# Optimization experiments

Measured on AMD Instinct MI355X. Metric: run time of the kernel, lower is better.

Reference implementation:

```python
import jax, jax.numpy as jnp
import numpy as np

IN, OUT, FP, B, S = 8192, 28672, 128, 32, 1


def setup_inputs() -> dict:
    key = jax.random.key(0)
    k = jax.random.split(key, 6)
    x = jax.random.normal(k[0], (B, S, IN), dtype=jnp.float32).astype(jnp.float16)
    # int8 quantized weight, stored as [OUT, IN]
    weight = jax.random.randint(k[1], (OUT, IN), -128, 128, dtype=jnp.int32).astype(jnp.int8)
    # per-output-column dequant scale (fp16, positive, small)
    scale_col = (jax.random.uniform(k[2], (1, OUT), dtype=jnp.float32) * 0.01 + 1e-4).astype(jnp.float16)
    # fp16 cache of the outlier weight columns [OUT, FP]
    weight_cache = (jax.random.normal(k[3], (OUT, FP), dtype=jnp.float32) * 0.02).astype(jnp.float16)
    bias = (jax.random.normal(k[4], (OUT,), dtype=jnp.float32) * 0.02).astype(jnp.float16)
    # sorted unique outlier column indices
    ind = jnp.sort(jax.random.permutation(k[5], IN)[:FP]).astype(jnp.int32)
    return {"x": x, "weight": weight, "scale_col": scale_col,
            "weight_cache": weight_cache, "bias": bias, "ind": ind}


def reference(x, weight, scale_col, weight_cache, bias, ind):
    out_features = weight.shape[0]
    shape = x.shape[:-1] + (out_features,)
    inputs = x.reshape(-1, x.shape[-1])                       # [M, IN] fp16
    # ExtractOutliersAndSetToZeros: gather outlier activation columns, zero them
    act_outliers = inputs[:, ind]                              # [M, FP] fp16
    tmp = inputs.at[:, ind].set(jnp.float16(0))                # [M, IN]
    # FindRowScale (bit=8): symmetric per-row int8 scale
    x_scale = jnp.max(jnp.abs(tmp), axis=1, keepdims=True) / jnp.float16(127)  # [M, 1]
    q_x = jnp.clip(jnp.round(tmp / x_scale), -128, 127).astype(jnp.int8)       # [M, IN]
    # int8FusedDequantize: int8 GEMM -> dequant with row/col scales -> add fp16 outlier GEMM
    y_int = jnp.matmul(q_x.astype(jnp.int32), weight.T.astype(jnp.int32))      # [M, OUT] int32
    y = y_int.astype(jnp.float16) * x_scale * scale_col                        # dequantize
    y = y + jnp.matmul(act_outliers, weight_cache.T)                           # outlier fp16 GEMM
    y = y + bias
    return y.reshape(shape)
```

## Files before the change

kernel.cpp:

```cpp
#include <hip/hip_runtime.h>
#include <hip/hip_fp16.h>

#define IN_F   8192
#define OUT_F  28672
#define NFP    128
#define NB     32
#define KQTOT  (IN_F / 4)

#define WS_QPK 0
#define WS_XS  262144
#define WS_ACT 263168

typedef int v4i  __attribute__((ext_vector_type(4)));
typedef int v16i __attribute__((ext_vector_type(16)));

__device__ __forceinline__ int pack8(int4 v) {
    return (v.x & 0xFF) | ((v.y & 0xFF) << 8) | ((v.z & 0xFF) << 16) | (v.w << 24);
}

__global__ __launch_bounds__(256) void quant_kernel(
    const float* __restrict__ x, const int* __restrict__ ind,
    int* __restrict__ q_pk, float* __restrict__ xs_out,
    float* __restrict__ act_out)
{
    __shared__ unsigned char flags[IN_F];
    __shared__ float redbuf[4];
    __shared__ float xs_sh;
    const int tid = threadIdx.x;
    const int b = blockIdx.x;

    int* fl4 = (int*)flags;
    for (int i = tid; i < IN_F / 4; i += 256) fl4[i] = 0;
    __syncthreads();
    if (tid < NFP) flags[ind[tid]] = 1;
    __syncthreads();

    const float* xrow = x + (size_t)b * IN_F;
    const float4* x4 = (const float4*)xrow;
    float mx = 0.f;
    for (int c = tid; c < IN_F / 4; c += 256) {
        float4 v = x4[c];
        int fw = fl4[c];
        if (!(fw & 0x000000FF)) mx = fmaxf(mx, fabsf(v.x));
        if (!(fw & 0x0000FF00)) mx = fmaxf(mx, fabsf(v.y));
        if (!(fw & 0x00FF0000)) mx = fmaxf(mx, fabsf(v.z));
        if (!(fw & 0xFF000000)) mx = fmaxf(mx, fabsf(v.w));
    }
    #pragma unroll
    for (int off = 32; off > 0; off >>= 1) {
        float o = __shfl_down(mx, off, 64);
        mx = o > mx ? o : mx;
    }
    if ((tid & 63) == 0) redbuf[tid >> 6] = mx;
    __syncthreads();
    if (tid == 0) {
        float m = redbuf[0];
        #pragma unroll
        for (int i = 1; i < 4; i++) m = redbuf[i] > m ? redbuf[i] : m;
        float xs = __half2float(__float2half_rn(m / 127.0f));
        xs_sh = xs;
        xs_out[b] = xs;
    }
    __syncthreads();
    const float xs = xs_sh;

    for (int c = tid; c < IN_F / 4; c += 256) {
        float4 v = x4[c];
        int fw = fl4[c];
        float ee[4];
        ee[0] = (fw & 0x000000FF) ? 0.f : v.x;
        ee[1] = (fw & 0x0000FF00) ? 0.f : v.y;
        ee[2] = (fw & 0x00FF0000) ? 0.f : v.z;
        ee[3] = (fw & 0xFF000000) ? 0.f : v.w;
        int pk = 0;
        #pragma unroll
        for (int j = 0; j < 4; j++) {
            float qf = __half2float(__float2half_rn(ee[j] / xs));
            float r = rintf(qf);
            r = fminf(fmaxf(r, -128.f), 127.f);
            int qi = (int)r;
            pk |= (qi & 0xFF) << (8 * j);
        }
        q_pk[(size_t)b * KQTOT + c] = pk;
    }
    if (tid < NFP) act_out[b * NFP + tid] = xrow[ind[tid]];
}

#define OT   64
#define KT   256
#define KQT  (KT / 4)
#define WROW 68
#define QROW 68

__global__ __launch_bounds__(128) void gemm_kernel(
    const int* __restrict__ w, const int* __restrict__ q_pk,
    const float* __restrict__ xs_ws, const float* __restrict__ act_ws,
    const float* __restrict__ sc, const float* __restrict__ wc,
    const float* __restrict__ bias, float* __restrict__ out)
{
    __shared__ int   w_p[OT * WROW] __attribute__((aligned(16)));
    __shared__ int   q_t[NB * QROW] __attribute__((aligned(16)));
    __shared__ float act_l[NB * NFP];
    __shared__ float xs_l[NB];

    const int tid  = threadIdx.x;
    const int wave = tid >> 6;
    const int lane = tid & 63;
    const int nl   = lane & 31;
    const int half = lane >> 5;

    const int blk_o = blockIdx.x * OT;
    const int n = blk_o + wave * 32 + nl;

    for (int i = tid; i < NB * NFP; i += 128) act_l[i] = act_ws[i];
    if (tid < NB) xs_l[tid] = xs_ws[tid];

    v16i acc;
    #pragma unroll
    for (int r = 0; r < 16; r++) acc[r] = 0;

    for (int k0 = 0; k0 < IN_F; k0 += KT) {
        __syncthreads();
        #pragma unroll 4
        for (int i = 0; i < 8; i++) {
            int u  = i * 128 + tid;
            int r  = u >> 4;
            int c4 = u & 15;
            const int* src = w + (size_t)(blk_o + r) * IN_F + k0 + c4 * 16;
            int4 a = *(const int4*)(src + 0);
            int4 b = *(const int4*)(src + 4);
            int4 c = *(const int4*)(src + 8);
            int4 d = *(const int4*)(src + 12);
            int4 pk = make_int4(pack8(a), pack8(b), pack8(c), pack8(d));
            *(int4*)&w_p[r * WROW + c4 * 4] = pk;
        }
        #pragma unroll
        for (int i = 0; i < 4; i++) {
            int u  = i * 128 + tid;
            int b  = u >> 4;
            int c4 = u & 15;
            int4 v = *(const int4*)(q_pk + (size_t)b * KQTOT + (k0 >> 2) + c4 * 4);
            *(int4*)&q_t[b * QROW + c4 * 4] = v;
        }
        __syncthreads();

        const int* qrow = &q_t[nl * QROW + half * 4];
        const int* wrow = &w_p[(wave * 32 + nl) * WROW + half * 4];
        #pragma unroll
        for (int s = 0; s < KT / 32; s++) {
            v4i a = *(const v4i*)(qrow + s * 8);
            v4i b = *(const v4i*)(wrow + s * 8);
            acc = __builtin_amdgcn_mfma_i32_32x32x32_i8(a, b, acc, 0, 0, 0);
        }
    }

    const float scn = sc[n];
    const float bin = bias[n];
    const float* wcn = wc + (size_t)n * NFP;

    float dots[16];
    #pragma unroll
    for (int r = 0; r < 16; r++) dots[r] = 0.f;

    for (int j = 0; j < NFP; j += 4) {
        float4 wv = *(const float4*)(wcn + j);
        #pragma unroll
        for (int r = 0; r < 16; r++) {
            int b = (r & 3) + 8 * (r >> 2) + 4 * half;
            float4 av = *(const float4*)(&act_l[b * NFP + j]);
            dots[r] += av.x * wv.x + av.y * wv.y + av.z * wv.z + av.w * wv.w;
        }
    }

    #pragma unroll
    for (int r = 0; r < 16; r++) {
        int b = (r & 3) + 8 * (r >> 2) + 4 * half;
        out[(size_t)b * OUT_F + n] = (float)acc[r] * xs_l[b] * scn + dots[r] + bin;
    }
}

extern "C" void kernel_launch(void* const* d_in, const int* in_sizes, int n_in,
                              void* d_out, int out_size, void* d_ws, size_t ws_size,
                              hipStream_t stream) {
    const float* x    = (const float*)d_in[0];
    const int*   wgt  = (const int*)d_in[1];
    const float* scol = (const float*)d_in[2];
    const float* wch  = (const float*)d_in[3];
    const float* bias = (const float*)d_in[4];
    const int*   ind  = (const int*)d_in[5];
    float* out = (float*)d_out;

    int*   q_pk = (int*)((char*)d_ws + WS_QPK);
    float* xs   = (float*)((char*)d_ws + WS_XS);
    float* act  = (float*)((char*)d_ws + WS_ACT);

    quant_kernel<<<NB, 256, 0, stream>>>(x, ind, q_pk, xs, act);
    gemm_kernel<<<OUT_F / OT, 128, 0, stream>>>(wgt, q_pk, xs, act, scol, wch, bias, out);
}
```

Baseline: 1.194 ms.

## Split-K the int8 GEMM with double-buffered LDS and a separate epilogue kernel

Result: no change. 1.212 ms (+1.5%).

```diff
diff --git a/kernel.cpp b/kernel.cpp
--- a/kernel.cpp
+++ b/kernel.cpp
@@ -7,9 +7,13 @@
 #define NB     32
 #define KQTOT  (IN_F / 4)
 
-#define WS_QPK 0
-#define WS_XS  262144
-#define WS_ACT 263168
+#define KC     4
+#define KCHUNK (IN_F / KC)
+
+#define WS_QPK  0
+#define WS_XS   262144
+#define WS_ACT  263168
+#define WS_PART 524288
 
 typedef int v4i  __attribute__((ext_vector_type(4)));
 typedef int v16i __attribute__((ext_vector_type(16)));
@@ -86,22 +90,47 @@
     if (tid < NFP) act_out[b * NFP + tid] = xrow[ind[tid]];
 }
 
-#define OT   64
-#define KT   256
-#define KQT  (KT / 4)
-#define WROW 68
-#define QROW 68
+#define OT    64
+#define KT    256
+#define KQT   (KT / 4)
+#define WROW  68
+#define QROW  68
+#define NTILE (KCHUNK / KT)
+
+__device__ __forceinline__ void stage_tiles(
+    const int* __restrict__ w, const int* __restrict__ q_pk,
+    int* __restrict__ wp, int* __restrict__ qt,
+    int tid, int blk_o, int k0)
+{
+    #pragma unroll 4
+    for (int i = 0; i < 8; i++) {
+        int u  = i * 128 + tid;
+        int r  = u >> 4;
+        int c4 = u & 15;
+        const int* src = w + (size_t)(blk_o + r) * IN_F + k0 + c4 * 16;
+        int4 a = *(const int4*)(src + 0);
+        int4 b = *(const int4*)(src + 4);
+        int4 c = *(const int4*)(src + 8);
+        int4 d = *(const int4*)(src + 12);
+        int4 pk = make_int4(pack8(a), pack8(b), pack8(c), pack8(d));
+        *(int4*)&wp[r * WROW + c4 * 4] = pk;
+    }
+    #pragma unroll
+    for (int i = 0; i < 4; i++) {
+        int u  = i * 128 + tid;
+        int bb = u >> 4;
+        int c4 = u & 15;
+        int4 v = *(const int4*)(q_pk + (size_t)bb * KQTOT + (k0 >> 2) + c4 * 4);
+        *(int4*)&qt[bb * QROW + c4 * 4] = v;
+    }
+}
 
 __global__ __launch_bounds__(128) void gemm_kernel(
     const int* __restrict__ w, const int* __restrict__ q_pk,
-    const float* __restrict__ xs_ws, const float* __restrict__ act_ws,
-    const float* __restrict__ sc, const float* __restrict__ wc,
-    const float* __restrict__ bias, float* __restrict__ out)
-{
-    __shared__ int   w_p[OT * WROW] __attribute__((aligned(16)));
-    __shared__ int   q_t[NB * QROW] __attribute__((aligned(16)));
-    __shared__ float act_l[NB * NFP];
-    __shared__ float xs_l[NB];
+    int* __restrict__ part)
+{
+    __shared__ int w_p[2][OT * WROW] __attribute__((aligned(16)));
+    __shared__ int q_t[2][NB * QROW] __attribute__((aligned(16)));
 
     const int tid  = threadIdx.x;
     const int wave = tid >> 6;
@@ -109,73 +138,84 @@
     const int nl   = lane & 31;
     const int half = lane >> 5;
 
-    const int blk_o = blockIdx.x * OT;
+    const int kc    = blockIdx.x & (KC - 1);
+    const int blk_o = (blockIdx.x >> 2) * OT;
+    const int kbase = kc * KCHUNK;
     const int n = blk_o + wave * 32 + nl;
 
-    for (int i = tid; i < NB * NFP; i += 128) act_l[i] = act_ws[i];
-    if (tid < NB) xs_l[tid] = xs_ws[tid];
-
     v16i acc;
     #pragma unroll
     for (int r = 0; r < 16; r++) acc[r] = 0;
 
-    for (int k0 = 0; k0 < IN_F; k0 += KT) {
-        __syncthreads();
-        #pragma unroll 4
-        for (int i = 0; i < 8; i++) {
-            int u  = i * 128 + tid;
-            int r  = u >> 4;
-            int c4 = u & 15;
-            const int* src = w + (size_t)(blk_o + r) * IN_F + k0 + c4 * 16;
-            int4 a = *(const int4*)(src + 0);
-            int4 b = *(const int4*)(src + 4);
-            int4 c = *(const int4*)(src + 8);
-            int4 d = *(const int4*)(src + 12);
-            int4 pk = make_int4(pack8(a), pack8(b), pack8(c), pack8(d));
-            *(int4*)&w_p[r * WROW + c4 * 4] = pk;
-        }
-        #pragma unroll
-        for (int i = 0; i < 4; i++) {
-            int u  = i * 128 + tid;
-            int b  = u >> 4;
-            int c4 = u & 15;
-            int4 v = *(const int4*)(q_pk + (size_t)b * KQTOT + (k0 >> 2) + c4 * 4);
-            *(int4*)&q_t[b * QROW + c4 * 4] = v;
-        }
-        __syncthreads();
-
-        const int* qrow = &q_t[nl * QROW + half * 4];
-        const int* wrow = &w_p[(wave * 32 + nl) * WROW + half * 4];
+    stage_tiles(w, q_pk, w_p[0], q_t[0], tid, blk_o, kbase);
+    __syncthreads();
+
+    for (int t = 0; t < NTILE; ++t) {
+        const int cur = t & 1;
+        if (t + 1 < NTILE)
+            stage_tiles(w, q_pk, w_p[cur ^ 1], q_t[cur ^ 1],
+                        tid, blk_o, kbase + (t + 1) * KT);
+
+        const int* qrow = &q_t[cur][nl * QROW + half * 4];
+        const int* wrow = &w_p[cur][(wave * 32 + nl) * WROW + half * 4];
         #pragma unroll
         for (int s = 0; s < KT / 32; s++) {
             v4i a = *(const v4i*)(qrow + s * 8);
             v4i b = *(const v4i*)(wrow + s * 8);
             acc = __builtin_amdgcn_mfma_i32_32x32x32_i8(a, b, acc, 0, 0, 0);
         }
-    }
-
+        __syncthreads();
+    }
+
+    #pragma unroll
+    for (int r = 0; r < 16; r++) {
+        int b = (r & 3) + 8 * (r >> 2) + 4 * half;
+        part[((size_t)kc * NB + b) * OUT_F + n] = acc[r];
+    }
+}
+
+__global__ __launch_bounds__(256) void epilogue_kernel(
+    const int* __restrict__ part, const float* __restrict__ xs_ws,
+    const float* __restrict__ act_ws, const float* __restrict__ sc,
+    const float* __restrict__ wc, const float* __restrict__ bias,
+    float* __restrict__ out)
+{
+    __shared__ float act_l[NB * NFP];
+    __shared__ float xs_l[NB];
+    const int tid = threadIdx.x;
+    const int blk_o = blockIdx.x * 64;
+
+    for (int i = tid; i < NB * NFP; i += 256) act_l[i] = act_ws[i];
+    if (tid < NB) xs_l[tid] = xs_ws[tid];
+    __syncthreads();
+
+    const int nl = tid & 63;
+    const int n  = blk_o + nl;
+    const int b0 = (tid >> 6) * 8;
     const float scn = sc[n];
     const float bin = bias[n];
     const float* wcn = wc + (size_t)n * NFP;
 
-    float dots[16];
-    #pragma unroll
-    for (int r = 0; r < 16; r++) dots[r] = 0.f;
-
-    for (int j = 0; j < NFP; j += 4) {
-        float4 wv = *(const float4*)(wcn + j);
-        #pragma unroll
-        for (int r = 0; r < 16; r++) {
-            int b = (r & 3) + 8 * (r >> 2) + 4 * half;
-            float4 av = *(const float4*)(&act_l[b * NFP + j]);
-            dots[r] += av.x * wv.x + av.y * wv.y + av.z * wv.z + av.w * wv.w;
+    float dots[8];
+    #pragma unroll
+    for (int j = 0; j < 8; j++) dots[j] = 0.f;
+    for (int u = 0; u < NFP; u += 4) {
+        float4 wv = *(const float4*)(wcn + u);
+        #pragma unroll
+        for (int j = 0; j < 8; j++) {
+            float4 av = *(const float4*)(&act_l[(b0 + j) * NFP + u]);
+            dots[j] += av.x * wv.x + av.y * wv.y + av.z * wv.z + av.w * wv.w;
         }
     }
 
     #pragma unroll
-    for (int r = 0; r < 16; r++) {
-        int b = (r & 3) + 8 * (r >> 2) + 4 * half;
-        out[(size_t)b * OUT_F + n] = (float)acc[r] * xs_l[b] * scn + dots[r] + bin;
+    for (int j = 0; j < 8; j++) {
+        const int b = b0 + j;
+        const size_t idx = (size_t)b * OUT_F + n;
+        int s = part[idx];
+        #pragma unroll
+        for (int k = 1; k < KC; k++) s += part[((size_t)k * NB + b) * OUT_F + n];
+        out[idx] = (float)s * xs_l[b] * scn + dots[j] + bin;
     }
 }
 
@@ -193,7 +233,9 @@
     int*   q_pk = (int*)((char*)d_ws + WS_QPK);
     float* xs   = (float*)((char*)d_ws + WS_XS);
     float* act  = (float*)((char*)d_ws + WS_ACT);
+    int*   part = (int*)((char*)d_ws + WS_PART);
 
     quant_kernel<<<NB, 256, 0, stream>>>(x, ind, q_pk, xs, act);
-    gemm_kernel<<<OUT_F / OT, 128, 0, stream>>>(wgt, q_pk, xs, act, scol, wch, bias, out);
-}
+    gemm_kernel<<<(OUT_F / OT) * KC, 128, 0, stream>>>(wgt, q_pk, part);
+    epilogue_kernel<<<OUT_F / 64, 256, 0, stream>>>(part, xs, act, scol, wch, bias, out);
+}
```

## Split K across wave pairs with LDS reduction and larger K tile

Applied to the files above, without the earlier changes.

Result: no change. 1.204 ms (+0.8%).

```diff
diff --git a/kernel.cpp b/kernel.cpp
--- a/kernel.cpp
+++ b/kernel.cpp
@@ -7,9 +7,9 @@
 #define NB     32
 #define KQTOT  (IN_F / 4)
 
-#define WS_QPK 0
-#define WS_XS  262144
-#define WS_ACT 263168
+#define WS_QPK  0
+#define WS_XS   262144
+#define WS_ACT  263168
 
 typedef int v4i  __attribute__((ext_vector_type(4)));
 typedef int v16i __attribute__((ext_vector_type(16)));
@@ -86,96 +86,110 @@
     if (tid < NFP) act_out[b * NFP + tid] = xrow[ind[tid]];
 }
 
-#define OT   64
-#define KT   256
-#define KQT  (KT / 4)
-#define WROW 68
-#define QROW 68
-
-__global__ __launch_bounds__(128) void gemm_kernel(
+#define KT    512
+#define NT    (IN_F / KT)
+#define WROW  132
+#define QROW  132
+
+__global__ __launch_bounds__(256) void gemm_kernel(
     const int* __restrict__ w, const int* __restrict__ q_pk,
     const float* __restrict__ xs_ws, const float* __restrict__ act_ws,
     const float* __restrict__ sc, const float* __restrict__ wc,
     const float* __restrict__ bias, float* __restrict__ out)
 {
-    __shared__ int   w_p[OT * WROW] __attribute__((aligned(16)));
-    __shared__ int   q_t[NB * QROW] __attribute__((aligned(16)));
-    __shared__ float act_l[NB * NFP];
-    __shared__ float xs_l[NB];
+    __shared__ int w_p[64 * WROW] __attribute__((aligned(16)));
+    __shared__ int q_t[32 * QROW] __attribute__((aligned(16)));
 
     const int tid  = threadIdx.x;
-    const int wave = tid >> 6;
+    const int wv   = tid >> 6;
     const int lane = tid & 63;
     const int nl   = lane & 31;
     const int half = lane >> 5;
-
-    const int blk_o = blockIdx.x * OT;
-    const int n = blk_o + wave * 32 + nl;
-
-    for (int i = tid; i < NB * NFP; i += 128) act_l[i] = act_ws[i];
-    if (tid < NB) xs_l[tid] = xs_ws[tid];
+    const int cg   = wv & 1;
+    const int kg   = wv >> 1;
+
+    const int blk_o = blockIdx.x * 64;
+    const int n = blk_o + cg * 32 + nl;
 
     v16i acc;
     #pragma unroll
     for (int r = 0; r < 16; r++) acc[r] = 0;
 
-    for (int k0 = 0; k0 < IN_F; k0 += KT) {
-        __syncthreads();
-        #pragma unroll 4
+    for (int t = 0; t < NT; ++t) {
+        const int k0 = t * KT;
+        #pragma unroll 2
         for (int i = 0; i < 8; i++) {
-            int u  = i * 128 + tid;
-            int r  = u >> 4;
-            int c4 = u & 15;
-            const int* src = w + (size_t)(blk_o + r) * IN_F + k0 + c4 * 16;
+            int u  = i * 256 + tid;
+            int r  = u >> 5;
+            int c8 = u & 31;
+            const int* src = w + (size_t)(blk_o + r) * IN_F + k0 + c8 * 16;
             int4 a = *(const int4*)(src + 0);
             int4 b = *(const int4*)(src + 4);
             int4 c = *(const int4*)(src + 8);
             int4 d = *(const int4*)(src + 12);
             int4 pk = make_int4(pack8(a), pack8(b), pack8(c), pack8(d));
-            *(int4*)&w_p[r * WROW + c4 * 4] = pk;
+            *(int4*)&w_p[r * WROW + c8 * 4] = pk;
         }
         #pragma unroll
         for (int i = 0; i < 4; i++) {
-            int u  = i * 128 + tid;
-            int b  = u >> 4;
-            int c4 = u & 15;
-            int4 v = *(const int4*)(q_pk + (size_t)b * KQTOT + (k0 >> 2) + c4 * 4);
-            *(int4*)&q_t[b * QROW + c4 * 4] = v;
+            int u  = i * 256 + tid;
+            int bb = u >> 5;
+            int c8 = u & 31;
+            int4 v = *(const int4*)(q_pk + (size_t)bb * KQTOT + (k0 >> 2) + c8 * 4);
+            *(int4*)&q_t[bb * QROW + c8 * 4] = v;
         }
         __syncthreads();
 
-        const int* qrow = &q_t[nl * QROW + half * 4];
-        const int* wrow = &w_p[(wave * 32 + nl) * WROW + half * 4];
-        #pragma unroll
-        for (int s = 0; s < KT / 32; s++) {
-            v4i a = *(const v4i*)(qrow + s * 8);
-            v4i b = *(const v4i*)(wrow + s * 8);
+        const int kd = kg * 64 + half * 4;
+        const int* qrow = &q_t[nl * QROW + kd];
+        const int* wrow = &w_p[(cg * 32 + nl) * WROW + kd];
+        #pragma unroll
+        for (int s = 0; s < 8; s++) {
+            v4i a = *(const v4i*)(qrow + 8 * s);
+            v4i b = *(const v4i*)(wrow + 8 * s);
             acc = __builtin_amdgcn_mfma_i32_32x32x32_i8(a, b, acc, 0, 0, 0);
         }
-    }
-
-    const float scn = sc[n];
-    const float bin = bias[n];
-    const float* wcn = wc + (size_t)n * NFP;
-
-    float dots[16];
-    #pragma unroll
-    for (int r = 0; r < 16; r++) dots[r] = 0.f;
-
-    for (int j = 0; j < NFP; j += 4) {
-        float4 wv = *(const float4*)(wcn + j);
+        __syncthreads();
+    }
+
+    int* red = q_t;
+    if (kg == 1) {
+        #pragma unroll
+        for (int r = 0; r < 16; r++) red[(cg * 64 + lane) * 16 + r] = acc[r];
+    }
+    float* act_l = (float*)w_p;
+    for (int i = tid; i < NB * NFP; i += 256) act_l[i] = act_ws[i];
+    float* xs_l = (float*)&q_t[2048];
+    if (tid < NB) xs_l[tid] = xs_ws[tid];
+    __syncthreads();
+
+    if (kg == 0) {
+        #pragma unroll
+        for (int r = 0; r < 16; r++) acc[r] += red[(cg * 64 + lane) * 16 + r];
+
+        const float scn = sc[n];
+        const float bin = bias[n];
+        const float* wcn = wc + (size_t)n * NFP;
+
+        float dots[16];
+        #pragma unroll
+        for (int r = 0; r < 16; r++) dots[r] = 0.f;
+
+        for (int j = 0; j < NFP; j += 4) {
+            float4 wv4 = *(const float4*)(wcn + j);
+            #pragma unroll
+            for (int r = 0; r < 16; r++) {
+                int b = (r & 3) + 8 * (r >> 2) + 4 * half;
+                float4 av = *(const float4*)(&act_l[b * NFP + j]);
+                dots[r] += av.x * wv4.x + av.y * wv4.y + av.z * wv4.z + av.w * wv4.w;
+            }
+        }
+
         #pragma unroll
         for (int r = 0; r < 16; r++) {
             int b = (r & 3) + 8 * (r >> 2) + 4 * half;
-            float4 av = *(const float4*)(&act_l[b * NFP + j]);
-            dots[r] += av.x * wv.x + av.y * wv.y + av.z * wv.z + av.w * wv.w;
-        }
-    }
-
-    #pragma unroll
-    for (int r = 0; r < 16; r++) {
-        int b = (r & 3) + 8 * (r >> 2) + 4 * half;
-        out[(size_t)b * OUT_F + n] = (float)acc[r] * xs_l[b] * scn + dots[r] + bin;
+            out[(size_t)b * OUT_F + n] = (float)acc[r] * xs_l[b] * scn + dots[r] + bin;
+        }
     }
 }
 
@@ -195,5 +209,5 @@
     float* act  = (float*)((char*)d_ws + WS_ACT);
 
     quant_kernel<<<NB, 256, 0, stream>>>(x, ind, q_pk, xs, act);
-    gemm_kernel<<<OUT_F / OT, 128, 0, stream>>>(wgt, q_pk, xs, act, scol, wch, bias, out);
-}
+    gemm_kernel<<<OUT_F / 64, 256, 0, stream>>>(wgt, q_pk, xs, act, scol, wch, bias, out);
+}
```
